# Performance work log

Hardware: AMD Instinct MI355X
Metric: run time of the kernel (lower is better)

## Reference

```python
import jax, jax.numpy as jnp
import numpy as np

DELTA_V = 0.5
DELTA_D = 3.0
PARAM_VAR = 1.0
PARAM_DIST = 1.0
PARAM_REG = 0.001
D = 4          # EMBEDDING_FEATS_DIMS; also num_segments for instance labels
H = 512
B = 32


def _safe_norm(x, axis):
    # L2 norm with grad-safe sqrt at 0 (forward value identical to torch.norm)
    sq = jnp.sum(x * x, axis=axis)
    nz = sq > 0
    return jnp.sqrt(jnp.where(nz, sq, 1.0)) * nz.astype(x.dtype)


def _single_disc_loss(emb, lab):
    # emb: [D, H, W] float; lab: [H, W] int in [0, D)
    x = emb.reshape(D, -1).T                     # [N, D] per-pixel embeddings
    seg = lab.reshape(-1)                        # [N]
    n = x.shape[0]
    ones = jnp.ones((n,), x.dtype)
    counts = jax.ops.segment_sum(ones, seg, num_segments=D)          # [D]
    counts_safe = jnp.where(counts > 0, counts, 1.0)                 # temp_count init'd to ones
    ssum = jax.ops.segment_sum(x, seg, num_segments=D)               # [D, D]
    ssum = ssum.at[0].set(0.0)                                       # zero background sum
    mu = ssum / counts_safe[:, None]                                 # [D, D]

    # variance term: hinge on per-pixel distance to own cluster mean
    dist = _safe_norm(mu[seg] - x, axis=1)                           # [N]
    dist = jnp.square(jnp.maximum(dist - DELTA_V, 0.0))
    dsum = jax.ops.segment_sum(dist, seg, num_segments=D)            # [D]
    present = (counts > 0).at[0].set(False)                          # instances 1..D-1 present
    presf = present.astype(x.dtype)
    npres = jnp.sum(presf)
    l_var = jnp.sum((dsum / counts_safe) * presf) / jnp.maximum(npres, 1.0)

    # distance term: pairwise mu hinge with zero-row masking (as in original)
    mu_i = jnp.repeat(mu, D, axis=0)                                 # [D*D, D] interleaved
    mu_b = jnp.tile(mu, (D, 1))                                      # [D*D, D] band
    mu_b = mu_b * (mu_i != 0).astype(x.dtype)
    mu_i = mu_i * (mu_b != 0).astype(x.dtype)
    diff = mu_b - mu_i
    mask = (jnp.sum(jnp.abs(diff), axis=1) != 0).astype(x.dtype)     # boolean_mask
    mn = jnp.square(jnp.maximum(2.0 * DELTA_D - _safe_norm(diff, axis=1), 0.0))
    msum = jnp.sum(mask)
    l_dist = jnp.where(msum > 0, jnp.sum(mn * mask) / jnp.maximum(msum, 1.0), 0.0)

    l_reg = jnp.mean(_safe_norm(mu, axis=1))

    loss = PARAM_VAR * l_var + PARAM_DIST * l_dist + PARAM_REG * l_reg
    # original returns 0.0 when no foreground instance exists
    return jnp.where(npres > 0, loss, 0.0)


def setup_inputs() -> dict:
    key = jax.random.key(0)
    k1, k2, k3 = jax.random.split(key, 3)
    pix_embedding = jax.random.normal(k1, (B, D, H, H), dtype=jnp.float32)
    y = jax.random.normal(k2, (B, 1, H, H), dtype=jnp.float32)
    instance_label = jax.random.randint(k3, (B, H, H), 0, D, dtype=jnp.int64)
    return {"pix_embedding": pix_embedding, "y": y, "instance_label": instance_label}


def reference(pix_embedding, y, instance_label):
    # y is unpacked from `inputs` in the original forward but never used
    losses = jax.vmap(_single_disc_loss)(pix_embedding, instance_label)
    return jnp.mean(losses)
```

## Files before the change

kernel.cpp:

```cpp
#include <hip/hip_runtime.h>
#include <math.h>

#define BATCH 32
#define HW    (512*512)
#define N4    (HW/4)
#define BPB   32
#define TPB   256

#define WS_SSUM   0
#define WS_DSUM   3072
#define WS_MU     3840
#define WS_LCONST 5376
#define WS_COUNTS 5504
#define WS_BYTES  6016

__device__ __forceinline__ float waveReduce(float v) {
#pragma unroll
  for (int off = 32; off > 0; off >>= 1) v += __shfl_down(v, off, 64);
  return v;
}

__global__ __launch_bounds__(TPB) void k_sums(const float* __restrict__ emb,
                                              const int*   __restrict__ lab,
                                              double*      __restrict__ ssum,
                                              unsigned int* __restrict__ counts) {
  const int b   = blockIdx.y;
  const int tid = threadIdx.x;
  const float4* e0 = (const float4*)emb + (size_t)(b*4 + 0) * N4;
  const float4* e1 = (const float4*)emb + (size_t)(b*4 + 1) * N4;
  const float4* e2 = (const float4*)emb + (size_t)(b*4 + 2) * N4;
  const float4* e3 = (const float4*)emb + (size_t)(b*4 + 3) * N4;
  const int4*   lp = (const int4*)lab + (size_t)b * N4;

  float s[3][4] = {{0.f,0.f,0.f,0.f},{0.f,0.f,0.f,0.f},{0.f,0.f,0.f,0.f}};
  unsigned c[4] = {0u,0u,0u,0u};

  for (int i = blockIdx.x * TPB + tid; i < N4; i += BPB * TPB) {
    float4 v0 = e0[i], v1 = e1[i], v2 = e2[i], v3 = e3[i];
    int4 l4 = lp[i];
    const int ls[4] = {l4.x, l4.y, l4.z, l4.w};
    const float xs[4][4] = {{v0.x,v1.x,v2.x,v3.x},{v0.y,v1.y,v2.y,v3.y},
                            {v0.z,v1.z,v2.z,v3.z},{v0.w,v1.w,v2.w,v3.w}};
#pragma unroll
    for (int k = 0; k < 4; k++) {
      int l = ls[k];
      c[0] += (l == 0); c[1] += (l == 1); c[2] += (l == 2); c[3] += (l == 3);
#pragma unroll
      for (int seg = 0; seg < 3; seg++) {
        float m = (l == seg + 1) ? 1.0f : 0.0f;
#pragma unroll
        for (int d = 0; d < 4; d++) s[seg][d] += m * xs[k][d];
      }
    }
  }

  __shared__ float red[4][16];
  int wave = tid >> 6, lane = tid & 63;
  float vals[16];
#pragma unroll
  for (int seg = 0; seg < 3; seg++)
#pragma unroll
    for (int d = 0; d < 4; d++) vals[seg*4 + d] = s[seg][d];
#pragma unroll
  for (int k = 0; k < 4; k++) vals[12 + k] = (float)c[k];
#pragma unroll
  for (int v = 0; v < 16; v++) {
    float r = waveReduce(vals[v]);
    if (lane == 0) red[wave][v] = r;
  }
  __syncthreads();
  if (tid < 16) {
    float t = red[0][tid] + red[1][tid] + red[2][tid] + red[3][tid];
    if (tid < 12) atomicAdd(&ssum[b*12 + tid], (double)t);
    else          atomicAdd(&counts[b*4 + (tid - 12)], (unsigned)(t + 0.5f));
  }
}

__global__ void k_mu(const double* __restrict__ ssum, const unsigned* __restrict__ counts,
                     float* __restrict__ muout, float* __restrict__ lconst) {
  int b = threadIdx.x;
  if (b >= BATCH) return;
  float mu[4][4];
#pragma unroll
  for (int c = 0; c < 4; c++) mu[0][c] = 0.f;
#pragma unroll
  for (int s = 1; s < 4; s++) {
    unsigned cnt = counts[b*4 + s];
    double cs = (cnt > 0) ? (double)cnt : 1.0;
#pragma unroll
    for (int c = 0; c < 4; c++) {
      float v = (float)(ssum[b*12 + (s-1)*4 + c] / cs);
      mu[s][c] = v;
      muout[b*12 + (s-1)*4 + c] = v;
    }
  }
  float mnsum = 0.f; int msum = 0;
#pragma unroll
  for (int i = 0; i < 4; i++) {
#pragma unroll
    for (int j = 0; j < 4; j++) {
      float sabs = 0.f, nsq = 0.f;
#pragma unroll
      for (int c = 0; c < 4; c++) {
        float bv = (mu[i][c] != 0.f) ? mu[j][c] : 0.f;
        float iv = (bv != 0.f) ? mu[i][c] : 0.f;
        float df = bv - iv;
        sabs += fabsf(df);
        nsq  += df * df;
      }
      if (sabs != 0.f) {
        msum += 1;
        float t = fmaxf(6.0f - sqrtf(nsq), 0.f);
        mnsum += t * t;
      }
    }
  }
  float l_dist = (msum > 0) ? (mnsum / (float)msum) : 0.f;
  float rs = 0.f;
#pragma unroll
  for (int s = 0; s < 4; s++) {
    float nsq = 0.f;
#pragma unroll
    for (int c = 0; c < 4; c++) nsq += mu[s][c] * mu[s][c];
    rs += sqrtf(nsq);
  }
  float l_reg = rs * 0.25f;
  lconst[b] = 1.0f * l_dist + 0.001f * l_reg;
}

__global__ __launch_bounds__(TPB) void k_var(const float* __restrict__ emb,
                                             const int*   __restrict__ lab,
                                             const float* __restrict__ mu,
                                             double*      __restrict__ dsum) {
  const int b   = blockIdx.y;
  const int tid = threadIdx.x;
  const float4* e0 = (const float4*)emb + (size_t)(b*4 + 0) * N4;
  const float4* e1 = (const float4*)emb + (size_t)(b*4 + 1) * N4;
  const float4* e2 = (const float4*)emb + (size_t)(b*4 + 2) * N4;
  const float4* e3 = (const float4*)emb + (size_t)(b*4 + 3) * N4;
  const int4*   lp = (const int4*)lab + (size_t)b * N4;

  float m1v[4], m2v[4], m3v[4];
#pragma unroll
  for (int c = 0; c < 4; c++) {
    m1v[c] = mu[b*12 + 0 + c];
    m2v[c] = mu[b*12 + 4 + c];
    m3v[c] = mu[b*12 + 8 + c];
  }
  float a1 = 0.f, a2 = 0.f, a3 = 0.f;

  for (int i = blockIdx.x * TPB + tid; i < N4; i += BPB * TPB) {
    float4 v0 = e0[i], v1 = e1[i], v2 = e2[i], v3 = e3[i];
    int4 l4 = lp[i];
    const int ls[4] = {l4.x, l4.y, l4.z, l4.w};
    const float xs[4][4] = {{v0.x,v1.x,v2.x,v3.x},{v0.y,v1.y,v2.y,v3.y},
                            {v0.z,v1.z,v2.z,v3.z},{v0.w,v1.w,v2.w,v3.w}};
#pragma unroll
    for (int k = 0; k < 4; k++) {
      int l = ls[k];
      float m1 = (l == 1) ? 1.f : 0.f;
      float m2 = (l == 2) ? 1.f : 0.f;
      float m3 = (l == 3) ? 1.f : 0.f;
      float d0 = xs[k][0] - (m1*m1v[0] + m2*m2v[0] + m3*m3v[0]);
      float d1 = xs[k][1] - (m1*m1v[1] + m2*m2v[1] + m3*m3v[1]);
      float d2 = xs[k][2] - (m1*m1v[2] + m2*m2v[2] + m3*m3v[2]);
      float d3 = xs[k][3] - (m1*m1v[3] + m2*m2v[3] + m3*m3v[3]);
      float dsq = d0*d0 + d1*d1 + d2*d2 + d3*d3;
      float h = fmaxf(sqrtf(dsq) - 0.5f, 0.f);
      float hh = h * h;
      a1 += hh * m1; a2 += hh * m2; a3 += hh * m3;
    }
  }

  __shared__ float red[4][3];
  int wave = tid >> 6, lane = tid & 63;
  float vals[3] = {a1, a2, a3};
#pragma unroll
  for (int v = 0; v < 3; v++) {
    float r = waveReduce(vals[v]);
    if (lane == 0) red[wave][v] = r;
  }
  __syncthreads();
  if (tid < 3) {
    float t = red[0][tid] + red[1][tid] + red[2][tid] + red[3][tid];
    atomicAdd(&dsum[b*3 + tid], (double)t);
  }
}

__global__ void k_final(const double* __restrict__ dsum, const unsigned* __restrict__ counts,
                        const float* __restrict__ lconst, float* __restrict__ out) {
  int tid = threadIdx.x;
  float loss = 0.f;
  if (tid < BATCH) {
    int npres = 0; float acc = 0.f;
#pragma unroll
    for (int s = 1; s < 4; s++) {
      unsigned cnt = counts[tid*4 + s];
      if (cnt > 0) { npres++; acc += (float)(dsum[tid*3 + (s-1)] / (double)cnt); }
    }
    float l_var = (npres > 0) ? acc / (float)npres : 0.f;
    loss = (npres > 0) ? (l_var + lconst[tid]) : 0.f;
  }
#pragma unroll
  for (int off = 32; off > 0; off >>= 1) loss += __shfl_down(loss, off, 64);
  if (tid == 0) out[0] = loss / (float)BATCH;
}

extern "C" void kernel_launch(void* const* d_in, const int* in_sizes, int n_in,
                              void* d_out, int out_size, void* d_ws, size_t ws_size,
                              hipStream_t stream) {
  const float* emb = (const float*)d_in[0];
  const int*   lab = (const int*)d_in[2];
  float* out = (float*)d_out;
  char* ws = (char*)d_ws;
  double*   ssum   = (double*)(ws + WS_SSUM);
  double*   dsum   = (double*)(ws + WS_DSUM);
  float*    mu     = (float*)(ws + WS_MU);
  float*    lconst = (float*)(ws + WS_LCONST);
  unsigned* counts = (unsigned*)(ws + WS_COUNTS);

  hipMemsetAsync(d_ws, 0, WS_BYTES, stream);

  dim3 grid(BPB, BATCH);
  k_sums<<<grid, TPB, 0, stream>>>(emb, lab, ssum, counts);
  k_mu  <<<1, 64, 0, stream>>>(ssum, counts, mu, lconst);
  k_var <<<grid, TPB, 0, stream>>>(emb, lab, mu, dsum);
  k_final<<<1, 64, 0, stream>>>(dsum, counts, lconst, out);
}
```

Baseline: 68.51 us.

## Fold mean and final-loss kernels into variance kernel via last-block reduction

Removes the two single-block launches (mean computation and final reduction). Each variance block now computes cluster means directly from the atomically accumulated sums and counts. A global done-counter picks the last finishing block to compute the distance, regularization and final loss. The background count is no longer accumulated and counts are tracked as floats. Two launches and their gaps go away, in exchange for a threadfence, an extra atomic per block and a small amount of redundant mean computation per block.

```diff
diff --git a/kernel.cpp b/kernel.cpp
--- a/kernel.cpp
+++ b/kernel.cpp
@@ -9,10 +9,9 @@
 
 #define WS_SSUM   0
 #define WS_DSUM   3072
-#define WS_MU     3840
-#define WS_LCONST 5376
-#define WS_COUNTS 5504
-#define WS_BYTES  6016
+#define WS_COUNTS 3840
+#define WS_DONE   4224
+#define WS_BYTES  4352
 
 __device__ __forceinline__ float waveReduce(float v) {
 #pragma unroll
@@ -32,8 +31,8 @@
   const float4* e3 = (const float4*)emb + (size_t)(b*4 + 3) * N4;
   const int4*   lp = (const int4*)lab + (size_t)b * N4;
 
-  float s[3][4] = {{0.f,0.f,0.f,0.f},{0.f,0.f,0.f,0.f},{0.f,0.f,0.f,0.f}};
-  unsigned c[4] = {0u,0u,0u,0u};
+  float s[3][4] = {{0,0,0,0},{0,0,0,0},{0,0,0,0}};
+  float c[3] = {0.f, 0.f, 0.f};
 
   for (int i = blockIdx.x * TPB + tid; i < N4; i += BPB * TPB) {
     float4 v0 = e0[i], v1 = e1[i], v2 = e2[i], v3 = e3[i];
@@ -44,111 +43,69 @@
 #pragma unroll
     for (int k = 0; k < 4; k++) {
       int l = ls[k];
-      c[0] += (l == 0); c[1] += (l == 1); c[2] += (l == 2); c[3] += (l == 3);
 #pragma unroll
       for (int seg = 0; seg < 3; seg++) {
         float m = (l == seg + 1) ? 1.0f : 0.0f;
+        c[seg] += m;
 #pragma unroll
         for (int d = 0; d < 4; d++) s[seg][d] += m * xs[k][d];
       }
     }
   }
 
-  __shared__ float red[4][16];
+  __shared__ float red[4][15];
   int wave = tid >> 6, lane = tid & 63;
-  float vals[16];
+  float vals[15];
 #pragma unroll
   for (int seg = 0; seg < 3; seg++)
 #pragma unroll
     for (int d = 0; d < 4; d++) vals[seg*4 + d] = s[seg][d];
 #pragma unroll
-  for (int k = 0; k < 4; k++) vals[12 + k] = (float)c[k];
-#pragma unroll
-  for (int v = 0; v < 16; v++) {
+  for (int k = 0; k < 3; k++) vals[12 + k] = c[k];
+#pragma unroll
+  for (int v = 0; v < 15; v++) {
     float r = waveReduce(vals[v]);
     if (lane == 0) red[wave][v] = r;
   }
   __syncthreads();
-  if (tid < 16) {
+  if (tid < 15) {
     float t = red[0][tid] + red[1][tid] + red[2][tid] + red[3][tid];
     if (tid < 12) atomicAdd(&ssum[b*12 + tid], (double)t);
-    else          atomicAdd(&counts[b*4 + (tid - 12)], (unsigned)(t + 0.5f));
-  }
-}
-
-__global__ void k_mu(const double* __restrict__ ssum, const unsigned* __restrict__ counts,
-                     float* __restrict__ muout, float* __restrict__ lconst) {
-  int b = threadIdx.x;
-  if (b >= BATCH) return;
-  float mu[4][4];
-#pragma unroll
-  for (int c = 0; c < 4; c++) mu[0][c] = 0.f;
-#pragma unroll
-  for (int s = 1; s < 4; s++) {
-    unsigned cnt = counts[b*4 + s];
-    double cs = (cnt > 0) ? (double)cnt : 1.0;
-#pragma unroll
-    for (int c = 0; c < 4; c++) {
-      float v = (float)(ssum[b*12 + (s-1)*4 + c] / cs);
-      mu[s][c] = v;
-      muout[b*12 + (s-1)*4 + c] = v;
-    }
-  }
-  float mnsum = 0.f; int msum = 0;
-#pragma unroll
-  for (int i = 0; i < 4; i++) {
-#pragma unroll
-    for (int j = 0; j < 4; j++) {
-      float sabs = 0.f, nsq = 0.f;
-#pragma unroll
-      for (int c = 0; c < 4; c++) {
-        float bv = (mu[i][c] != 0.f) ? mu[j][c] : 0.f;
-        float iv = (bv != 0.f) ? mu[i][c] : 0.f;
-        float df = bv - iv;
-        sabs += fabsf(df);
-        nsq  += df * df;
-      }
-      if (sabs != 0.f) {
-        msum += 1;
-        float t = fmaxf(6.0f - sqrtf(nsq), 0.f);
-        mnsum += t * t;
-      }
-    }
-  }
-  float l_dist = (msum > 0) ? (mnsum / (float)msum) : 0.f;
-  float rs = 0.f;
-#pragma unroll
-  for (int s = 0; s < 4; s++) {
-    float nsq = 0.f;
-#pragma unroll
-    for (int c = 0; c < 4; c++) nsq += mu[s][c] * mu[s][c];
-    rs += sqrtf(nsq);
-  }
-  float l_reg = rs * 0.25f;
-  lconst[b] = 1.0f * l_dist + 0.001f * l_reg;
+    else          atomicAdd(&counts[b*3 + (tid - 12)], (unsigned)(t + 0.5f));
+  }
 }
 
 __global__ __launch_bounds__(TPB) void k_var(const float* __restrict__ emb,
                                              const int*   __restrict__ lab,
-                                             const float* __restrict__ mu,
-                                             double*      __restrict__ dsum) {
+                                             double*      __restrict__ ssum,
+                                             unsigned int* __restrict__ counts,
+                                             double*      __restrict__ dsum,
+                                             unsigned int* __restrict__ done,
+                                             float*       __restrict__ out) {
   const int b   = blockIdx.y;
   const int tid = threadIdx.x;
+
+  float m1v[4], m2v[4], m3v[4];
+  {
+    unsigned c1 = counts[b*3+0], c2 = counts[b*3+1], c3 = counts[b*3+2];
+    double s1 = (c1 > 0) ? (double)c1 : 1.0;
+    double s2 = (c2 > 0) ? (double)c2 : 1.0;
+    double s3 = (c3 > 0) ? (double)c3 : 1.0;
+#pragma unroll
+    for (int cc = 0; cc < 4; cc++) {
+      m1v[cc] = (float)(ssum[b*12 + 0 + cc] / s1);
+      m2v[cc] = (float)(ssum[b*12 + 4 + cc] / s2);
+      m3v[cc] = (float)(ssum[b*12 + 8 + cc] / s3);
+    }
+  }
+
   const float4* e0 = (const float4*)emb + (size_t)(b*4 + 0) * N4;
   const float4* e1 = (const float4*)emb + (size_t)(b*4 + 1) * N4;
   const float4* e2 = (const float4*)emb + (size_t)(b*4 + 2) * N4;
   const float4* e3 = (const float4*)emb + (size_t)(b*4 + 3) * N4;
   const int4*   lp = (const int4*)lab + (size_t)b * N4;
 
-  float m1v[4], m2v[4], m3v[4];
-#pragma unroll
-  for (int c = 0; c < 4; c++) {
-    m1v[c] = mu[b*12 + 0 + c];
-    m2v[c] = mu[b*12 + 4 + c];
-    m3v[c] = mu[b*12 + 8 + c];
-  }
   float a1 = 0.f, a2 = 0.f, a3 = 0.f;
-
   for (int i = blockIdx.x * TPB + tid; i < N4; i += BPB * TPB) {
     float4 v0 = e0[i], v1 = e1[i], v2 = e2[i], v3 = e3[i];
     int4 l4 = lp[i];
@@ -173,6 +130,7 @@
   }
 
   __shared__ float red[4][3];
+  __shared__ bool last;
   int wave = tid >> 6, lane = tid & 63;
   float vals[3] = {a1, a2, a3};
 #pragma unroll
@@ -185,21 +143,74 @@
     float t = red[0][tid] + red[1][tid] + red[2][tid] + red[3][tid];
     atomicAdd(&dsum[b*3 + tid], (double)t);
   }
-}
-
-__global__ void k_final(const double* __restrict__ dsum, const unsigned* __restrict__ counts,
-                        const float* __restrict__ lconst, float* __restrict__ out) {
-  int tid = threadIdx.x;
+  __threadfence();
+  if (tid == 0) {
+    unsigned prev = atomicAdd(done, 1u);
+    last = (prev == (unsigned)(BPB * BATCH - 1));
+  }
+  __syncthreads();
+  if (!last) return;
+
   float loss = 0.f;
   if (tid < BATCH) {
+    int bb = tid;
+    unsigned cn[3]; double ds[3]; double ss[12];
+#pragma unroll
+    for (int k = 0; k < 3; k++) {
+      cn[k] = atomicAdd(&counts[bb*3 + k], 0u);
+      ds[k] = atomicAdd(&dsum[bb*3 + k], 0.0);
+    }
+#pragma unroll
+    for (int k = 0; k < 12; k++) ss[k] = atomicAdd(&ssum[bb*12 + k], 0.0);
+
+    float mu[4][4];
+#pragma unroll
+    for (int cc = 0; cc < 4; cc++) mu[0][cc] = 0.f;
+#pragma unroll
+    for (int s = 1; s < 4; s++) {
+      double cs = (cn[s-1] > 0) ? (double)cn[s-1] : 1.0;
+#pragma unroll
+      for (int cc = 0; cc < 4; cc++) mu[s][cc] = (float)(ss[(s-1)*4 + cc] / cs);
+    }
+    float mnsum = 0.f; int msum = 0;
+#pragma unroll
+    for (int i = 0; i < 4; i++) {
+#pragma unroll
+      for (int j = 0; j < 4; j++) {
+        float sabs = 0.f, nsq = 0.f;
+#pragma unroll
+        for (int cc = 0; cc < 4; cc++) {
+          float bv = (mu[i][cc] != 0.f) ? mu[j][cc] : 0.f;
+          float iv = (bv != 0.f) ? mu[i][cc] : 0.f;
+          float df = bv - iv;
+          sabs += fabsf(df);
+          nsq  += df * df;
+        }
+        if (sabs != 0.f) {
+          msum += 1;
+          float t = fmaxf(6.0f - sqrtf(nsq), 0.f);
+          mnsum += t * t;
+        }
+      }
+    }
+    float l_dist = (msum > 0) ? (mnsum / (float)msum) : 0.f;
+    float rs = 0.f;
+#pragma unroll
+    for (int s = 0; s < 4; s++) {
+      float nsq = 0.f;
+#pragma unroll
+      for (int cc = 0; cc < 4; cc++) nsq += mu[s][cc] * mu[s][cc];
+      rs += sqrtf(nsq);
+    }
+    float lconst = l_dist + 0.001f * (rs * 0.25f);
+
     int npres = 0; float acc = 0.f;
 #pragma unroll
-    for (int s = 1; s < 4; s++) {
-      unsigned cnt = counts[tid*4 + s];
-      if (cnt > 0) { npres++; acc += (float)(dsum[tid*3 + (s-1)] / (double)cnt); }
+    for (int s = 0; s < 3; s++) {
+      if (cn[s] > 0) { npres++; acc += (float)(ds[s] / (double)cn[s]); }
     }
     float l_var = (npres > 0) ? acc / (float)npres : 0.f;
-    loss = (npres > 0) ? (l_var + lconst[tid]) : 0.f;
+    loss = (npres > 0) ? (l_var + lconst) : 0.f;
   }
 #pragma unroll
   for (int off = 32; off > 0; off >>= 1) loss += __shfl_down(loss, off, 64);
@@ -215,15 +226,12 @@
   char* ws = (char*)d_ws;
   double*   ssum   = (double*)(ws + WS_SSUM);
   double*   dsum   = (double*)(ws + WS_DSUM);
-  float*    mu     = (float*)(ws + WS_MU);
-  float*    lconst = (float*)(ws + WS_LCONST);
   unsigned* counts = (unsigned*)(ws + WS_COUNTS);
+  unsigned* done   = (unsigned*)(ws + WS_DONE);
 
   hipMemsetAsync(d_ws, 0, WS_BYTES, stream);
 
   dim3 grid(BPB, BATCH);
   k_sums<<<grid, TPB, 0, stream>>>(emb, lab, ssum, counts);
-  k_mu  <<<1, 64, 0, stream>>>(ssum, counts, mu, lconst);
-  k_var <<<grid, TPB, 0, stream>>>(emb, lab, mu, dsum);
-  k_final<<<1, 64, 0, stream>>>(dsum, counts, lconst, out);
-}
+  k_var <<<grid, TPB, 0, stream>>>(emb, lab, ssum, counts, dsum, done, out);
+}
```

Measured after the change: 169.3 us. 147% more time.
